# Kernel tuning notes

Hardware: AMD Instinct MI355X
Metric: run time of the kernel (lower is better)

## Reference

```python
import jax, jax.numpy as jnp
import numpy as np

D_MODEL = 1024
NUM_HEADS = 16
HEAD_DIM = D_MODEL // NUM_HEADS
THETA = 10000.0
MAX_SEQ_LEN = 2048
BATCH = 4
SEQ = 2048


def _rope_tables():
    # theta_vec = 1 / theta**(arange(0, d_k, 2)/d_k), pos outer product
    inv_freq = 1.0 / (THETA ** (jnp.arange(0, HEAD_DIM, 2, dtype=jnp.float32) / HEAD_DIM))
    pos = jnp.arange(MAX_SEQ_LEN, dtype=jnp.float32)
    freqs = jnp.outer(pos, inv_freq)  # [max_seq, head_dim//2]
    return jnp.cos(freqs), jnp.sin(freqs)


def apply_rope(x, cos, sin):
    # x: [..., S, d]; cos/sin: [S, d//2]; interleaved pairwise rotation
    x1 = x[..., 0::2]
    x2 = x[..., 1::2]
    o1 = x1 * cos - x2 * sin
    o2 = x2 * cos + x1 * sin
    return jnp.stack([o1, o2], axis=-1).reshape(x.shape)


def setup_inputs() -> dict:
    key = jax.random.key(0)
    kx, kq, kk, kv, ko = jax.random.split(key, 5)
    std = (1.0 / D_MODEL) ** 0.5
    x = jax.random.normal(kx, (BATCH, SEQ, D_MODEL), dtype=jnp.float32)
    w_q = jax.random.normal(kq, (D_MODEL, D_MODEL), dtype=jnp.float32) * std
    w_k = jax.random.normal(kk, (D_MODEL, D_MODEL), dtype=jnp.float32) * std
    w_v = jax.random.normal(kv, (D_MODEL, D_MODEL), dtype=jnp.float32) * std
    w_o = jax.random.normal(ko, (D_MODEL, D_MODEL), dtype=jnp.float32) * std
    cos, sin = _rope_tables()
    return {"x": x, "w_q": w_q, "w_k": w_k, "w_v": w_v, "w_o": w_o,
            "cos": cos, "sin": sin}


def reference(x, w_q, w_k, w_v, w_o, cos, sin):
    b, s, d = x.shape
    h, dk = NUM_HEADS, HEAD_DIM

    def proj(w):
        # einsum '... s d, hd d -> ... s hd' == x @ w.T, then split heads
        y = jnp.einsum('bsd,ed->bse', x, w)
        return y.reshape(b, s, h, dk).transpose(0, 2, 1, 3)  # [b,h,s,dk]

    q = apply_rope(proj(w_q), cos[:s], sin[:s])
    k = apply_rope(proj(w_k), cos[:s], sin[:s])
    v = proj(w_v)

    scores = jnp.einsum('bhnd,bhmd->bhnm', q, k) / (dk ** 0.5)
    causal = jnp.tril(jnp.ones((s, s), dtype=bool))
    scores = jnp.where(causal, scores, -jnp.inf)
    attn = jax.nn.softmax(scores, axis=-1)
    out = jnp.einsum('bhnm,bhmd->bhnd', attn, v)  # [b,h,s,dk]
    out = out.transpose(0, 2, 1, 3).reshape(b, s, d)
    # einsum '... s hd, d hd -> ... s d' == out @ w_o.T
    return jnp.einsum('bse,de->bsd', out, w_o)
```

## Files before the change

kernel.cpp:

```cpp
#include <hip/hip_runtime.h>
#include <hip/hip_bf16.h>


typedef __bf16 bf16;
typedef __bf16 bf16x8 __attribute__((ext_vector_type(8)));
typedef __bf16 bf16x4 __attribute__((ext_vector_type(4)));
typedef float f32x4 __attribute__((ext_vector_type(4)));

#define LOG2E 1.4426950408889634f
#define ATTN_C1 (0.125f * LOG2E)
#define ATTN_C2 (16.0f * LOG2E)

__device__ __forceinline__ void async16(const void* g, void* l) {
  __builtin_amdgcn_global_load_lds(
      (const __attribute__((address_space(1))) void*)g,
      (__attribute__((address_space(3))) void*)l, 16, 0, 0);
}

__global__ void cast_all_kernel(const float* __restrict__ x,
                                const float* __restrict__ wq,
                                const float* __restrict__ wk,
                                const float* __restrict__ wv,
                                const float* __restrict__ wo,
                                bf16* __restrict__ xb, bf16* __restrict__ wb) {
  int i = blockIdx.x * blockDim.x + threadIdx.x;
  const float* src;
  bf16* dst;
  long o;
  if (i < 2097152) {
    src = x; dst = xb; o = i;
  } else {
    long j = i - 2097152;
    int w = (int)(j >> 18);
    o = j & 262143;
    src = (w == 0) ? wq : (w == 1) ? wk : (w == 2) ? wv : wo;
    dst = wb + (long)w * 1048576;
  }
  float4 v = reinterpret_cast<const float4*>(src)[o];
  bf16x4 out;
  out.x = (bf16)v.x; out.y = (bf16)v.y; out.z = (bf16)v.z; out.w = (bf16)v.w;
  *reinterpret_cast<bf16x4*>(dst + o * 4) = out;
}

template <int EPI>
__global__ __launch_bounds__(256) void gemm_bt(const bf16* __restrict__ A,
                                               const bf16* __restrict__ B,
                                               void* __restrict__ C, int M,
                                               int N, int K) {
  __shared__ __align__(16) bf16 As[128 * 32];
  __shared__ __align__(16) bf16 Bs[128 * 32];
  const int tid = threadIdx.x;
  const int wid = tid >> 6, lane = tid & 63;
  const int quad = lane >> 4, l15 = lane & 15;
  const int waveM = wid >> 1, waveN = wid & 1;
  const int bm = blockIdx.y, bn = blockIdx.x;

  f32x4 acc[4][4] = {};

  const bf16* Ag = A + (long)bm * 128 * K;
  const bf16* Bg = B + (long)bn * 128 * K;

  for (int k0 = 0; k0 < K; k0 += 32) {
#pragma unroll
    for (int it = 0; it < 2; ++it) {
      int chunk = it * 256 + tid;
      int r = chunk >> 2;
      int c = ((chunk & 3) ^ (r & 3)) << 3;
      int ldsbase = (it * 256 + wid * 64) * 16;
      async16(Ag + (long)r * K + k0 + c, (char*)As + ldsbase);
      async16(Bg + (long)r * K + k0 + c, (char*)Bs + ldsbase);
    }
    __syncthreads();
    bf16x8 af[4], bfr[4];
#pragma unroll
    for (int t = 0; t < 4; ++t) {
      int rowA = waveM * 64 + t * 16 + l15;
      af[t] = *(const bf16x8*)(As + rowA * 32 + ((quad ^ (rowA & 3)) << 3));
    }
#pragma unroll
    for (int t = 0; t < 4; ++t) {
      int rowB = waveN * 64 + t * 16 + l15;
      bfr[t] = *(const bf16x8*)(Bs + rowB * 32 + ((quad ^ (rowB & 3)) << 3));
    }
#pragma unroll
    for (int mt = 0; mt < 4; ++mt)
#pragma unroll
      for (int nt = 0; nt < 4; ++nt)
        acc[mt][nt] = __builtin_amdgcn_mfma_f32_16x16x32_bf16(
            af[mt], bfr[nt], acc[mt][nt], 0, 0, 0);
    __syncthreads();
  }

#pragma unroll
  for (int mt = 0; mt < 4; ++mt)
#pragma unroll
    for (int nt = 0; nt < 4; ++nt)
#pragma unroll
      for (int r = 0; r < 4; ++r) {
        int row = bm * 128 + waveM * 64 + mt * 16 + quad * 4 + r;
        int col = bn * 128 + waveN * 64 + nt * 16 + l15;
        float v = acc[mt][nt][r];
        if (EPI == 1) {
          long off = (long)(col >> 11) * 2097152 + (long)row * 2048 +
                     (col & 2047);
          ((bf16*)C)[off] = (bf16)v;
        } else {
          ((float*)C)[(long)row * N + col] = v;
        }
      }
}

__global__ __launch_bounds__(256) void gemm_qk(const bf16* __restrict__ A,
                                               const bf16* __restrict__ B,
                                               bf16* __restrict__ QK,
                                               const float* __restrict__ cosT,
                                               const float* __restrict__ sinT,
                                               int K) {
  __shared__ __align__(16) bf16 As[128 * 32];
  __shared__ __align__(16) bf16 Bs[128 * 32];
  const int tid = threadIdx.x;
  const int wid = tid >> 6, lane = tid & 63;
  const int quad = lane >> 4, l15 = lane & 15;
  const int waveM = wid >> 1, waveN = wid & 1;
  const int bm = blockIdx.y, bn = blockIdx.x;

  f32x4 acc[4][4] = {};
  const bf16* Ag = A + (long)bm * 128 * K;
  const bf16* Bg = B + (long)bn * 128 * K;

  for (int k0 = 0; k0 < K; k0 += 32) {
#pragma unroll
    for (int it = 0; it < 2; ++it) {
      int chunk = it * 256 + tid;
      int r = chunk >> 2;
      int c = ((chunk & 3) ^ (r & 3)) << 3;
      int ldsbase = (it * 256 + wid * 64) * 16;
      async16(Ag + (long)r * K + k0 + c, (char*)As + ldsbase);
      async16(Bg + (long)r * K + k0 + c, (char*)Bs + ldsbase);
    }
    __syncthreads();
    bf16x8 af[4], bfr[4];
#pragma unroll
    for (int t = 0; t < 4; ++t) {
      int rowA = waveM * 64 + t * 16 + l15;
      af[t] = *(const bf16x8*)(As + rowA * 32 + ((quad ^ (rowA & 3)) << 3));
    }
#pragma unroll
    for (int t = 0; t < 4; ++t) {
      int rowB = waveN * 64 + t * 16 + l15;
      bfr[t] = *(const bf16x8*)(Bs + rowB * 32 + ((quad ^ (rowB & 3)) << 3));
    }
#pragma unroll
    for (int mt = 0; mt < 4; ++mt)
#pragma unroll
      for (int nt = 0; nt < 4; ++nt)
        acc[mt][nt] = __builtin_amdgcn_mfma_f32_16x16x32_bf16(
            af[mt], bfr[nt], acc[mt][nt], 0, 0, 0);
    __syncthreads();
  }

#pragma unroll
  for (int mt = 0; mt < 4; ++mt)
#pragma unroll
    for (int nt = 0; nt < 4; ++nt)
#pragma unroll
      for (int r = 0; r < 4; ++r) {
        int row = bm * 128 + waveM * 64 + mt * 16 + quad * 4 + r;
        int col = bn * 128 + waveN * 64 + nt * 16 + l15;
        float v = acc[mt][nt][r];
        float pr = __shfl_xor(v, 1);
        int d = col & 63;
        int ti = (row & 2047) * 32 + (d >> 1);
        float c = cosT[ti], sn = sinT[ti];
        float o = (col & 1) ? (v * c + pr * sn) : (v * c - pr * sn);
        long off = (long)(col >> 10) * 8388608 +
                   (long)(((row >> 11) << 4) + ((col >> 6) & 15)) * 131072 +
                   (long)(row & 2047) * 64 + d;
        QK[off] = (bf16)o;
      }
}

__device__ __forceinline__ void attn_step(const bf16* Ks, const bf16* Vs,
                                          bf16* Pw, const bf16x8* qf,
                                          f32x4* accO, float& lsum, int quad,
                                          int l15, int qloc, bool diag) {
  const int sw = l15 & 7;
  f32x4 sacc[4] = {};
#pragma unroll
  for (int mt = 0; mt < 4; ++mt)
#pragma unroll
    for (int kk = 0; kk < 2; ++kk) {
      bf16x8 kf = *(const bf16x8*)(Ks + (mt * 16 + l15) * 64 +
                                   ((((kk << 2) + quad) ^ sw) << 3));
      sacc[mt] =
          __builtin_amdgcn_mfma_f32_16x16x32_bf16(kf, qf[kk], sacc[mt], 0, 0, 0);
    }
  if (diag) {
#pragma unroll
    for (int mt = 0; mt < 4; ++mt)
#pragma unroll
      for (int r = 0; r < 4; ++r)
        if ((mt * 16 + quad * 4 + r) > qloc) sacc[mt][r] = -__builtin_inff();
  }
  bf16x4 pk[4];
#pragma unroll
  for (int mt = 0; mt < 4; ++mt)
#pragma unroll
    for (int r = 0; r < 4; ++r) {
      float p = exp2f(fmaf(sacc[mt][r], ATTN_C1, -ATTN_C2));
      lsum += p;
      pk[mt][r] = (bf16)p;
    }
#pragma unroll
  for (int mt = 0; mt < 4; ++mt)
    *(bf16x4*)(Pw + l15 * 88 + mt * 16 + quad * 4) = pk[mt];
  asm volatile("s_waitcnt lgkmcnt(0)" ::: "memory");
  bf16x8 pfr[2];
#pragma unroll
  for (int kk = 0; kk < 2; ++kk)
    pfr[kk] = *(const bf16x8*)(Pw + l15 * 88 + kk * 32 + quad * 8);
#pragma unroll
  for (int nt = 0; nt < 4; ++nt)
#pragma unroll
    for (int kk = 0; kk < 2; ++kk) {
      bf16x8 vf = *(const bf16x8*)(Vs + (nt * 16 + l15) * 64 +
                                   ((((kk << 2) + quad) ^ sw) << 3));
      accO[nt] =
          __builtin_amdgcn_mfma_f32_16x16x32_bf16(pfr[kk], vf, accO[nt], 0, 0, 0);
    }
}

__global__ __launch_bounds__(256, 4) void attn_kernel(
    const bf16* __restrict__ Q, const bf16* __restrict__ Kg,
    const bf16* __restrict__ VT, bf16* __restrict__ Out) {
  __shared__ __align__(16) bf16 Ks[64 * 64];
  __shared__ __align__(16) bf16 Vs[64 * 64];
  __shared__ __align__(16) bf16 Ps[4][16 * 88];
  const int tid = threadIdx.x, wid = tid >> 6, lane = tid & 63;
  const int quad = lane >> 4, l15 = lane & 15;
  const int p = blockIdx.x, bh = blockIdx.y;
  const int q0t = p, q1t = 31 - p;
  const bf16* Qb = Q + (long)bh * 131072;
  const bf16* Kb = Kg + (long)bh * 131072;
  const bf16* Vb = VT + (long)bh * 131072;
  bf16* Pw = &Ps[wid][0];
  const int qloc = wid * 16 + l15;

  bf16x8 qf0[2], qf1[2];
#pragma unroll
  for (int kk = 0; kk < 2; ++kk) {
    qf0[kk] = *(const bf16x8*)(Qb + (long)(q0t * 64 + qloc) * 64 + kk * 32 +
                               quad * 8);
    qf1[kk] = *(const bf16x8*)(Qb + (long)(q1t * 64 + qloc) * 64 + kk * 32 +
                               quad * 8);
  }
  f32x4 acc0[4] = {}, acc1[4] = {};
  float l0 = 0.f, l1 = 0.f;

  for (int kt = 0; kt <= q1t; ++kt) {
#pragma unroll
    for (int it = 0; it < 2; ++it) {
      int chunk = it * 256 + tid;
      int r = chunk >> 3;
      int c = (((chunk & 7) ^ (r & 7)) << 3);
      int ldsbase = (it * 256 + wid * 64) * 16;
      async16(Kb + (long)(kt * 64 + r) * 64 + c, (char*)Ks + ldsbase);
      async16(Vb + (long)r * 2048 + kt * 64 + c, (char*)Vs + ldsbase);
    }
    __syncthreads();
    attn_step(Ks, Vs, Pw, qf1, acc1, l1, quad, l15, qloc, kt == q1t);
    if (kt <= q0t)
      attn_step(Ks, Vs, Pw, qf0, acc0, l0, quad, l15, qloc, kt == q0t);
    __syncthreads();
  }

  l0 += __shfl_xor(l0, 16); l0 += __shfl_xor(l0, 32);
  l1 += __shfl_xor(l1, 16); l1 += __shfl_xor(l1, 32);
  float rl0 = 1.0f / l0, rl1 = 1.0f / l1;

  const int b = bh >> 4, h = bh & 15;
#pragma unroll
  for (int r = 0; r < 4; ++r) {
    float lr0 = __shfl(rl0, quad * 4 + r);
    float lr1 = __shfl(rl1, quad * 4 + r);
#pragma unroll
    for (int nt = 0; nt < 4; ++nt) {
      int d = h * 64 + nt * 16 + l15;
      int qg0 = q0t * 64 + wid * 16 + quad * 4 + r;
      int qg1 = q1t * 64 + wid * 16 + quad * 4 + r;
      Out[(long)(b * 2048 + qg0) * 1024 + d] = (bf16)(acc0[nt][r] * lr0);
      Out[(long)(b * 2048 + qg1) * 1024 + d] = (bf16)(acc1[nt][r] * lr1);
    }
  }
}

extern "C" void kernel_launch(void* const* d_in, const int* in_sizes, int n_in,
                              void* d_out, int out_size, void* d_ws,
                              size_t ws_size, hipStream_t stream) {
  const float* x = (const float*)d_in[0];
  const float* w_q = (const float*)d_in[1];
  const float* w_k = (const float*)d_in[2];
  const float* w_v = (const float*)d_in[3];
  const float* w_o = (const float*)d_in[4];
  const float* cosT = (const float*)d_in[5];
  const float* sinT = (const float*)d_in[6];

  char* ws = (char*)d_ws;
  bf16* xb = (bf16*)(ws + 0);
  bf16* wqb = (bf16*)(ws + 16777216);
  bf16* wvb = (bf16*)(ws + 20971520);
  bf16* wob = (bf16*)(ws + 23068672);
  bf16* Qb = (bf16*)(ws + 25165824);
  bf16* Kb = (bf16*)(ws + 41943040);
  bf16* VTb = (bf16*)(ws + 58720256);
  bf16* attnb = xb;

  cast_all_kernel<<<12288, 256, 0, stream>>>(x, w_q, w_k, w_v, w_o, xb, wqb);

  gemm_qk<<<dim3(16, 64), 256, 0, stream>>>(xb, wqb, Qb, cosT, sinT, 1024);
  gemm_bt<1><<<dim3(64, 8), 256, 0, stream>>>(wvb, xb, VTb, 1024, 8192, 1024);

  attn_kernel<<<dim3(16, 64), 256, 0, stream>>>(Qb, Kb, VTb, attnb);

  gemm_bt<2><<<dim3(8, 64), 256, 0, stream>>>(attnb, wob, (float*)d_out, 8192,
                                              1024, 1024);
}
```

Baseline: 290.5 us.

## Double-buffer attention K/V tiles, fuse dual Q-tile steps, shrink GEMM tiles

The attention loop now double-buffers the K/V tiles in LDS, issuing the async load for the next tile before computing the current one. This removes one barrier per iteration and overlaps global loads with MFMA work. The two query tiles share each K fragment load, and the P scratch buffer is shrunk to 64 columns with an XOR swizzle instead of padding. The V and output-projection GEMMs move to a templated kernel with smaller 64x128 and 128x64 tiles, which doubles the block count and improves CU fill. The cost is more LDS per attention block, which may reduce occupancy, and more per-block overhead in the GEMMs.

```diff
diff --git a/kernel.cpp b/kernel.cpp
--- a/kernel.cpp
+++ b/kernel.cpp
@@ -16,6 +16,8 @@
       (const __attribute__((address_space(1))) void*)g,
       (__attribute__((address_space(3))) void*)l, 16, 0, 0);
 }
+
+#define MFMA16(a, b, c) __builtin_amdgcn_mfma_f32_16x16x32_bf16(a, b, c, 0, 0, 0)
 
 __global__ void cast_all_kernel(const float* __restrict__ x,
                                 const float* __restrict__ wq,
@@ -42,63 +44,71 @@
   *reinterpret_cast<bf16x4*>(dst + o * 4) = out;
 }
 
-template <int EPI>
-__global__ __launch_bounds__(256) void gemm_bt(const bf16* __restrict__ A,
-                                               const bf16* __restrict__ B,
-                                               void* __restrict__ C, int M,
-                                               int N, int K) {
-  __shared__ __align__(16) bf16 As[128 * 32];
-  __shared__ __align__(16) bf16 Bs[128 * 32];
+template <int EPI, int TM, int TN>
+__global__ __launch_bounds__(256) void gemm_tile(const bf16* __restrict__ A,
+                                                 const bf16* __restrict__ B,
+                                                 void* __restrict__ C, int N,
+                                                 int K) {
+  constexpr int WM = TM / 64;
+  constexpr int WN = 4 / WM;
+  constexpr int CW = TN / WN;
+  constexpr int NT = CW / 16;
+  constexpr int ROUNDS = (TM + TN) / 64;
+  __shared__ __align__(16) bf16 As[TM * 32];
+  __shared__ __align__(16) bf16 Bs[TN * 32];
   const int tid = threadIdx.x;
   const int wid = tid >> 6, lane = tid & 63;
   const int quad = lane >> 4, l15 = lane & 15;
-  const int waveM = wid >> 1, waveN = wid & 1;
+  const int waveM = wid / WN, waveN = wid % WN;
   const int bm = blockIdx.y, bn = blockIdx.x;
 
-  f32x4 acc[4][4] = {};
-
-  const bf16* Ag = A + (long)bm * 128 * K;
-  const bf16* Bg = B + (long)bn * 128 * K;
+  f32x4 acc[4][NT] = {};
+
+  const bf16* Ag = A + (long)bm * TM * K;
+  const bf16* Bg = B + (long)bn * TN * K;
 
   for (int k0 = 0; k0 < K; k0 += 32) {
 #pragma unroll
-    for (int it = 0; it < 2; ++it) {
-      int chunk = it * 256 + tid;
-      int r = chunk >> 2;
-      int c = ((chunk & 3) ^ (r & 3)) << 3;
-      int ldsbase = (it * 256 + wid * 64) * 16;
-      async16(Ag + (long)r * K + k0 + c, (char*)As + ldsbase);
-      async16(Bg + (long)r * K + k0 + c, (char*)Bs + ldsbase);
-    }
-    __syncthreads();
-    bf16x8 af[4], bfr[4];
+    for (int ri = 0; ri < ROUNDS; ++ri) {
+      int c = ri * 256 + tid;
+      int g = ri * 256 + (wid << 6);
+      bool isA = g < TM * 4;
+      int cl = isA ? c : c - TM * 4;
+      int r = cl >> 2;
+      int col = ((cl & 3) ^ (r & 3)) << 3;
+      const bf16* src = (isA ? Ag : Bg) + (long)r * K + k0 + col;
+      char* dst = isA ? ((char*)As + (long)g * 16)
+                      : ((char*)Bs + (long)(g - TM * 4) * 16);
+      async16(src, dst);
+    }
+    __syncthreads();
+    bf16x8 af[4], bfr[NT];
 #pragma unroll
     for (int t = 0; t < 4; ++t) {
       int rowA = waveM * 64 + t * 16 + l15;
       af[t] = *(const bf16x8*)(As + rowA * 32 + ((quad ^ (rowA & 3)) << 3));
     }
 #pragma unroll
-    for (int t = 0; t < 4; ++t) {
-      int rowB = waveN * 64 + t * 16 + l15;
+    for (int t = 0; t < NT; ++t) {
+      int rowB = waveN * CW + t * 16 + l15;
       bfr[t] = *(const bf16x8*)(Bs + rowB * 32 + ((quad ^ (rowB & 3)) << 3));
     }
 #pragma unroll
     for (int mt = 0; mt < 4; ++mt)
 #pragma unroll
-      for (int nt = 0; nt < 4; ++nt)
-        acc[mt][nt] = __builtin_amdgcn_mfma_f32_16x16x32_bf16(
-            af[mt], bfr[nt], acc[mt][nt], 0, 0, 0);
+      for (int nt = 0; nt < NT; ++nt)
+        acc[mt][nt] = MFMA16(af[mt], bfr[nt], acc[mt][nt]);
     __syncthreads();
   }
 
 #pragma unroll
   for (int mt = 0; mt < 4; ++mt)
 #pragma unroll
-    for (int nt = 0; nt < 4; ++nt)
+    for (int nt = 0; nt < NT; ++nt)
 #pragma unroll
       for (int r = 0; r < 4; ++r) {
-        int row = bm * 128 + waveM * 64 + mt * 16 + quad * 4 + r;
-        int col = bn * 128 + waveN * 64 + nt * 16 + l15;
+        int row = bm * TM + waveM * 64 + mt * 16 + quad * 4 + r;
+        int col = bn * TN + waveN * CW + nt * 16 + l15;
         float v = acc[mt][nt][r];
         if (EPI == 1) {
           long off = (long)(col >> 11) * 2097152 + (long)row * 2048 +
@@ -154,8 +164,7 @@
     for (int mt = 0; mt < 4; ++mt)
 #pragma unroll
       for (int nt = 0; nt < 4; ++nt)
-        acc[mt][nt] = __builtin_amdgcn_mfma_f32_16x16x32_bf16(
-            af[mt], bfr[nt], acc[mt][nt], 0, 0, 0);
+        acc[mt][nt] = MFMA16(af[mt], bfr[nt], acc[mt][nt]);
     __syncthreads();
   }
 
@@ -180,62 +189,12 @@
       }
 }
 
-__device__ __forceinline__ void attn_step(const bf16* Ks, const bf16* Vs,
-                                          bf16* Pw, const bf16x8* qf,
-                                          f32x4* accO, float& lsum, int quad,
-                                          int l15, int qloc, bool diag) {
-  const int sw = l15 & 7;
-  f32x4 sacc[4] = {};
-#pragma unroll
-  for (int mt = 0; mt < 4; ++mt)
-#pragma unroll
-    for (int kk = 0; kk < 2; ++kk) {
-      bf16x8 kf = *(const bf16x8*)(Ks + (mt * 16 + l15) * 64 +
-                                   ((((kk << 2) + quad) ^ sw) << 3));
-      sacc[mt] =
-          __builtin_amdgcn_mfma_f32_16x16x32_bf16(kf, qf[kk], sacc[mt], 0, 0, 0);
-    }
-  if (diag) {
-#pragma unroll
-    for (int mt = 0; mt < 4; ++mt)
-#pragma unroll
-      for (int r = 0; r < 4; ++r)
-        if ((mt * 16 + quad * 4 + r) > qloc) sacc[mt][r] = -__builtin_inff();
-  }
-  bf16x4 pk[4];
-#pragma unroll
-  for (int mt = 0; mt < 4; ++mt)
-#pragma unroll
-    for (int r = 0; r < 4; ++r) {
-      float p = exp2f(fmaf(sacc[mt][r], ATTN_C1, -ATTN_C2));
-      lsum += p;
-      pk[mt][r] = (bf16)p;
-    }
-#pragma unroll
-  for (int mt = 0; mt < 4; ++mt)
-    *(bf16x4*)(Pw + l15 * 88 + mt * 16 + quad * 4) = pk[mt];
-  asm volatile("s_waitcnt lgkmcnt(0)" ::: "memory");
-  bf16x8 pfr[2];
-#pragma unroll
-  for (int kk = 0; kk < 2; ++kk)
-    pfr[kk] = *(const bf16x8*)(Pw + l15 * 88 + kk * 32 + quad * 8);
-#pragma unroll
-  for (int nt = 0; nt < 4; ++nt)
-#pragma unroll
-    for (int kk = 0; kk < 2; ++kk) {
-      bf16x8 vf = *(const bf16x8*)(Vs + (nt * 16 + l15) * 64 +
-                                   ((((kk << 2) + quad) ^ sw) << 3));
-      accO[nt] =
-          __builtin_amdgcn_mfma_f32_16x16x32_bf16(pfr[kk], vf, accO[nt], 0, 0, 0);
-    }
-}
-
 __global__ __launch_bounds__(256, 4) void attn_kernel(
     const bf16* __restrict__ Q, const bf16* __restrict__ Kg,
     const bf16* __restrict__ VT, bf16* __restrict__ Out) {
-  __shared__ __align__(16) bf16 Ks[64 * 64];
-  __shared__ __align__(16) bf16 Vs[64 * 64];
-  __shared__ __align__(16) bf16 Ps[4][16 * 88];
+  __shared__ __align__(16) bf16 Ks[2][64 * 64];
+  __shared__ __align__(16) bf16 Vs[2][64 * 64];
+  __shared__ __align__(16) bf16 Ps[4][16 * 64];
   const int tid = threadIdx.x, wid = tid >> 6, lane = tid & 63;
   const int quad = lane >> 4, l15 = lane & 15;
   const int p = blockIdx.x, bh = blockIdx.y;
@@ -245,6 +204,8 @@
   const bf16* Vb = VT + (long)bh * 131072;
   bf16* Pw = &Ps[wid][0];
   const int qloc = wid * 16 + l15;
+  const int sw = l15 & 7;
+  const int psw = (l15 & 7) << 3;
 
   bf16x8 qf0[2], qf1[2];
 #pragma unroll
@@ -257,21 +218,120 @@
   f32x4 acc0[4] = {}, acc1[4] = {};
   float l0 = 0.f, l1 = 0.f;
 
-  for (int kt = 0; kt <= q1t; ++kt) {
+  auto stage = [&](int kt, int b) {
 #pragma unroll
     for (int it = 0; it < 2; ++it) {
       int chunk = it * 256 + tid;
       int r = chunk >> 3;
       int c = (((chunk & 7) ^ (r & 7)) << 3);
       int ldsbase = (it * 256 + wid * 64) * 16;
-      async16(Kb + (long)(kt * 64 + r) * 64 + c, (char*)Ks + ldsbase);
-      async16(Vb + (long)r * 2048 + kt * 64 + c, (char*)Vs + ldsbase);
-    }
-    __syncthreads();
-    attn_step(Ks, Vs, Pw, qf1, acc1, l1, quad, l15, qloc, kt == q1t);
-    if (kt <= q0t)
-      attn_step(Ks, Vs, Pw, qf0, acc0, l0, quad, l15, qloc, kt == q0t);
-    __syncthreads();
+      async16(Kb + (long)(kt * 64 + r) * 64 + c, (char*)Ks[b] + ldsbase);
+      async16(Vb + (long)r * 2048 + kt * 64 + c, (char*)Vs[b] + ldsbase);
+    }
+  };
+
+  stage(0, 0);
+  int cur = 0;
+  for (int kt = 0; kt <= q1t; ++kt, cur ^= 1) {
+    __syncthreads();
+    if (kt < q1t) stage(kt + 1, cur ^ 1);
+    const bf16* Kc = Ks[cur];
+    const bf16* Vc = Vs[cur];
+    const bool dual = (kt <= q0t);
+
+    f32x4 s1[4] = {}, s0[4] = {};
+    if (dual) {
+#pragma unroll
+      for (int mt = 0; mt < 4; ++mt)
+#pragma unroll
+        for (int kk = 0; kk < 2; ++kk) {
+          bf16x8 kf = *(const bf16x8*)(Kc + (mt * 16 + l15) * 64 +
+                                       ((((kk << 2) + quad) ^ sw) << 3));
+          s1[mt] = MFMA16(kf, qf1[kk], s1[mt]);
+          s0[mt] = MFMA16(kf, qf0[kk], s0[mt]);
+        }
+    } else {
+#pragma unroll
+      for (int mt = 0; mt < 4; ++mt)
+#pragma unroll
+        for (int kk = 0; kk < 2; ++kk) {
+          bf16x8 kf = *(const bf16x8*)(Kc + (mt * 16 + l15) * 64 +
+                                       ((((kk << 2) + quad) ^ sw) << 3));
+          s1[mt] = MFMA16(kf, qf1[kk], s1[mt]);
+        }
+    }
+    if (kt == q1t) {
+#pragma unroll
+      for (int mt = 0; mt < 4; ++mt)
+#pragma unroll
+        for (int r = 0; r < 4; ++r)
+          if ((mt * 16 + quad * 4 + r) > qloc) s1[mt][r] = -__builtin_inff();
+    }
+    if (dual && kt == q0t) {
+#pragma unroll
+      for (int mt = 0; mt < 4; ++mt)
+#pragma unroll
+        for (int r = 0; r < 4; ++r)
+          if ((mt * 16 + quad * 4 + r) > qloc) s0[mt][r] = -__builtin_inff();
+    }
+
+    bf16x4 pk1[4], pk0[4];
+#pragma unroll
+    for (int mt = 0; mt < 4; ++mt)
+#pragma unroll
+      for (int r = 0; r < 4; ++r) {
+        float pv = exp2f(fmaf(s1[mt][r], ATTN_C1, -ATTN_C2));
+        l1 += pv;
+        pk1[mt][r] = (bf16)pv;
+      }
+    if (dual) {
+#pragma unroll
+      for (int mt = 0; mt < 4; ++mt)
+#pragma unroll
+        for (int r = 0; r < 4; ++r) {
+          float pv = exp2f(fmaf(s0[mt][r], ATTN_C1, -ATTN_C2));
+          l0 += pv;
+          pk0[mt][r] = (bf16)pv;
+        }
+    }
+
+#pragma unroll
+    for (int mt = 0; mt < 4; ++mt)
+      *(bf16x4*)(Pw + l15 * 64 + ((mt * 16 + quad * 4) ^ psw)) = pk1[mt];
+    asm volatile("s_waitcnt lgkmcnt(0)" ::: "memory");
+    bf16x8 pf1[2];
+#pragma unroll
+    for (int kk = 0; kk < 2; ++kk)
+      pf1[kk] = *(const bf16x8*)(Pw + l15 * 64 + ((kk * 32 + quad * 8) ^ psw));
+    if (dual) {
+#pragma unroll
+      for (int mt = 0; mt < 4; ++mt)
+        *(bf16x4*)(Pw + l15 * 64 + ((mt * 16 + quad * 4) ^ psw)) = pk0[mt];
+    }
+#pragma unroll
+    for (int nt = 0; nt < 4; ++nt)
+#pragma unroll
+      for (int kk = 0; kk < 2; ++kk) {
+        bf16x8 vf = *(const bf16x8*)(Vc + (nt * 16 + l15) * 64 +
+                                     ((((kk << 2) + quad) ^ sw) << 3));
+        acc1[nt] = MFMA16(pf1[kk], vf, acc1[nt]);
+      }
+    if (dual) {
+      asm volatile("s_waitcnt lgkmcnt(0)" ::: "memory");
+      bf16x8 pf0[2];
+#pragma unroll
+      for (int kk = 0; kk < 2; ++kk)
+        pf0[kk] =
+            *(const bf16x8*)(Pw + l15 * 64 + ((kk * 32 + quad * 8) ^ psw));
+#pragma unroll
+      for (int nt = 0; nt < 4; ++nt)
+#pragma unroll
+        for (int kk = 0; kk < 2; ++kk) {
+          bf16x8 vf = *(const bf16x8*)(Vc + (nt * 16 + l15) * 64 +
+                                       ((((kk << 2) + quad) ^ sw) << 3));
+          acc0[nt] = MFMA16(pf0[kk], vf, acc0[nt]);
+        }
+    }
   }
 
   l0 += __shfl_xor(l0, 16); l0 += __shfl_xor(l0, 32);
@@ -318,10 +378,12 @@
   cast_all_kernel<<<12288, 256, 0, stream>>>(x, w_q, w_k, w_v, w_o, xb, wqb);
 
   gemm_qk<<<dim3(16, 64), 256, 0, stream>>>(xb, wqb, Qb, cosT, sinT, 1024);
-  gemm_bt<1><<<dim3(64, 8), 256, 0, stream>>>(wvb, xb, VTb, 1024, 8192, 1024);
+  gemm_tile<1, 64, 128><<<dim3(64, 16), 256, 0, stream>>>(wvb, xb, VTb, 8192,
+                                                          1024);
 
   attn_kernel<<<dim3(16, 64), 256, 0, stream>>>(Qb, Kb, VTb, attnb);
 
-  gemm_bt<2><<<dim3(8, 64), 256, 0, stream>>>(attnb, wob, (float*)d_out, 8192,
-                                              1024, 1024);
-}
+  gemm_tile<2, 128, 64><<<dim3(16, 64), 256, 0, stream>>>(attnb, wob,
+                                                          (float*)d_out, 1024,
+                                                          1024);
+}
```

New measurement: 294.2 us. No clear change (+1.3%).

## Replace softmax exp with bit-trick exponent, MFMA row sums, smaller GEMM tiles

Applied to the files above, without the earlier changes.

Q is pre-scaled by 2^23·log2e/8 in the QK projection epilogue, and the score accumulator is seeded with a bias constant. The float-to-int conversion of each score then directly yields the bit pattern of an approximate exp2, so the exp2f and fmaf calls per score are dropped and the bf16 packing becomes a byte permute. Row sums are now computed by an extra MFMA of P against a ones vector instead of scalar adds and cross-lane shuffles. The V and output projection GEMMs move to 64x128 and 128x64 tiles so they launch twice as many blocks. The Schraudolph-style exponent approximation adds error and relies on scores staying within a bounded range.

```diff
diff --git a/kernel.cpp b/kernel.cpp
--- a/kernel.cpp
+++ b/kernel.cpp
@@ -8,14 +8,16 @@
 typedef float f32x4 __attribute__((ext_vector_type(4)));
 
 #define LOG2E 1.4426950408889634f
-#define ATTN_C1 (0.125f * LOG2E)
-#define ATTN_C2 (16.0f * LOG2E)
+#define QSCALE (0.125f * LOG2E * 8388608.0f)
+#define SEXP_SEED ((126.94269504f - 16.0f * LOG2E) * 8388608.0f)
 
 __device__ __forceinline__ void async16(const void* g, void* l) {
   __builtin_amdgcn_global_load_lds(
       (const __attribute__((address_space(1))) void*)g,
       (__attribute__((address_space(3))) void*)l, 16, 0, 0);
 }
+
+#define MFMA16(a, b, c) __builtin_amdgcn_mfma_f32_16x16x32_bf16(a, b, c, 0, 0, 0)
 
 __global__ void cast_all_kernel(const float* __restrict__ x,
                                 const float* __restrict__ wq,
@@ -42,63 +44,71 @@
   *reinterpret_cast<bf16x4*>(dst + o * 4) = out;
 }
 
-template <int EPI>
-__global__ __launch_bounds__(256) void gemm_bt(const bf16* __restrict__ A,
-                                               const bf16* __restrict__ B,
-                                               void* __restrict__ C, int M,
-                                               int N, int K) {
-  __shared__ __align__(16) bf16 As[128 * 32];
-  __shared__ __align__(16) bf16 Bs[128 * 32];
+template <int EPI, int TM, int TN>
+__global__ __launch_bounds__(256) void gemm_tile(const bf16* __restrict__ A,
+                                                 const bf16* __restrict__ B,
+                                                 void* __restrict__ C, int N,
+                                                 int K) {
+  constexpr int WM = TM / 64;
+  constexpr int WN = 4 / WM;
+  constexpr int CW = TN / WN;
+  constexpr int NT = CW / 16;
+  constexpr int ROUNDS = (TM + TN) / 64;
+  __shared__ __align__(16) bf16 As[TM * 32];
+  __shared__ __align__(16) bf16 Bs[TN * 32];
   const int tid = threadIdx.x;
   const int wid = tid >> 6, lane = tid & 63;
   const int quad = lane >> 4, l15 = lane & 15;
-  const int waveM = wid >> 1, waveN = wid & 1;
+  const int waveM = wid / WN, waveN = wid % WN;
   const int bm = blockIdx.y, bn = blockIdx.x;
 
-  f32x4 acc[4][4] = {};
-
-  const bf16* Ag = A + (long)bm * 128 * K;
-  const bf16* Bg = B + (long)bn * 128 * K;
+  f32x4 acc[4][NT] = {};
+
+  const bf16* Ag = A + (long)bm * TM * K;
+  const bf16* Bg = B + (long)bn * TN * K;
 
   for (int k0 = 0; k0 < K; k0 += 32) {
 #pragma unroll
-    for (int it = 0; it < 2; ++it) {
-      int chunk = it * 256 + tid;
-      int r = chunk >> 2;
-      int c = ((chunk & 3) ^ (r & 3)) << 3;
-      int ldsbase = (it * 256 + wid * 64) * 16;
-      async16(Ag + (long)r * K + k0 + c, (char*)As + ldsbase);
-      async16(Bg + (long)r * K + k0 + c, (char*)Bs + ldsbase);
-    }
-    __syncthreads();
-    bf16x8 af[4], bfr[4];
+    for (int ri = 0; ri < ROUNDS; ++ri) {
+      int c = ri * 256 + tid;
+      int g = ri * 256 + (wid << 6);
+      bool isA = g < TM * 4;
+      int cl = isA ? c : c - TM * 4;
+      int r = cl >> 2;
+      int col = ((cl & 3) ^ (r & 3)) << 3;
+      const bf16* src = (isA ? Ag : Bg) + (long)r * K + k0 + col;
+      char* dst = isA ? ((char*)As + (long)g * 16)
+                      : ((char*)Bs + (long)(g - TM * 4) * 16);
+      async16(src, dst);
+    }
+    __syncthreads();
+    bf16x8 af[4], bfr[NT];
 #pragma unroll
     for (int t = 0; t < 4; ++t) {
       int rowA = waveM * 64 + t * 16 + l15;
       af[t] = *(const bf16x8*)(As + rowA * 32 + ((quad ^ (rowA & 3)) << 3));
     }
 #pragma unroll
-    for (int t = 0; t < 4; ++t) {
-      int rowB = waveN * 64 + t * 16 + l15;
+    for (int t = 0; t < NT; ++t) {
+      int rowB = waveN * CW + t * 16 + l15;
       bfr[t] = *(const bf16x8*)(Bs + rowB * 32 + ((quad ^ (rowB & 3)) << 3));
     }
 #pragma unroll
     for (int mt = 0; mt < 4; ++mt)
 #pragma unroll
-      for (int nt = 0; nt < 4; ++nt)
-        acc[mt][nt] = __builtin_amdgcn_mfma_f32_16x16x32_bf16(
-            af[mt], bfr[nt], acc[mt][nt], 0, 0, 0);
+      for (int nt = 0; nt < NT; ++nt)
+        acc[mt][nt] = MFMA16(af[mt], bfr[nt], acc[mt][nt]);
     __syncthreads();
   }
 
 #pragma unroll
   for (int mt = 0; mt < 4; ++mt)
 #pragma unroll
-    for (int nt = 0; nt < 4; ++nt)
+    for (int nt = 0; nt < NT; ++nt)
 #pragma unroll
       for (int r = 0; r < 4; ++r) {
-        int row = bm * 128 + waveM * 64 + mt * 16 + quad * 4 + r;
-        int col = bn * 128 + waveN * 64 + nt * 16 + l15;
+        int row = bm * TM + waveM * 64 + mt * 16 + quad * 4 + r;
+        int col = bn * TN + waveN * CW + nt * 16 + l15;
         float v = acc[mt][nt][r];
         if (EPI == 1) {
           long off = (long)(col >> 11) * 2097152 + (long)row * 2048 +
@@ -154,11 +164,11 @@
     for (int mt = 0; mt < 4; ++mt)
 #pragma unroll
       for (int nt = 0; nt < 4; ++nt)
-        acc[mt][nt] = __builtin_amdgcn_mfma_f32_16x16x32_bf16(
-            af[mt], bfr[nt], acc[mt][nt], 0, 0, 0);
-    __syncthreads();
-  }
-
+        acc[mt][nt] = MFMA16(af[mt], bfr[nt], acc[mt][nt]);
+    __syncthreads();
+  }
+
+  const float qsc = (bn < 8) ? QSCALE : 1.0f;
 #pragma unroll
   for (int mt = 0; mt < 4; ++mt)
 #pragma unroll
@@ -173,6 +183,7 @@
         int ti = (row & 2047) * 32 + (d >> 1);
         float c = cosT[ti], sn = sinT[ti];
         float o = (col & 1) ? (v * c + pr * sn) : (v * c - pr * sn);
+        o *= qsc;
         long off = (long)(col >> 10) * 8388608 +
                    (long)(((row >> 11) << 4) + ((col >> 6) & 15)) * 131072 +
                    (long)(row & 2047) * 64 + d;
@@ -182,38 +193,36 @@
 
 __device__ __forceinline__ void attn_step(const bf16* Ks, const bf16* Vs,
                                           bf16* Pw, const bf16x8* qf,
-                                          f32x4* accO, float& lsum, int quad,
-                                          int l15, int qloc, bool diag) {
+                                          const bf16x8 ones, f32x4* accO,
+                                          f32x4& accL, int quad, int l15,
+                                          int qloc, bool diag) {
   const int sw = l15 & 7;
-  f32x4 sacc[4] = {};
+  const f32x4 seedv = {SEXP_SEED, SEXP_SEED, SEXP_SEED, SEXP_SEED};
+  f32x4 sacc[4] = {seedv, seedv, seedv, seedv};
 #pragma unroll
   for (int mt = 0; mt < 4; ++mt)
 #pragma unroll
     for (int kk = 0; kk < 2; ++kk) {
       bf16x8 kf = *(const bf16x8*)(Ks + (mt * 16 + l15) * 64 +
                                    ((((kk << 2) + quad) ^ sw) << 3));
-      sacc[mt] =
-          __builtin_amdgcn_mfma_f32_16x16x32_bf16(kf, qf[kk], sacc[mt], 0, 0, 0);
+      sacc[mt] = MFMA16(kf, qf[kk], sacc[mt]);
     }
   if (diag) {
 #pragma unroll
     for (int mt = 0; mt < 4; ++mt)
 #pragma unroll
       for (int r = 0; r < 4; ++r)
-        if ((mt * 16 + quad * 4 + r) > qloc) sacc[mt][r] = -__builtin_inff();
-  }
-  bf16x4 pk[4];
-#pragma unroll
-  for (int mt = 0; mt < 4; ++mt)
-#pragma unroll
-    for (int r = 0; r < 4; ++r) {
-      float p = exp2f(fmaf(sacc[mt][r], ATTN_C1, -ATTN_C2));
-      lsum += p;
-      pk[mt][r] = (bf16)p;
-    }
-#pragma unroll
-  for (int mt = 0; mt < 4; ++mt)
-    *(bf16x4*)(Pw + l15 * 88 + mt * 16 + quad * 4) = pk[mt];
+        if ((mt * 16 + quad * 4 + r) > qloc) sacc[mt][r] = 0.0f;
+  }
+#pragma unroll
+  for (int mt = 0; mt < 4; ++mt) {
+    int i0 = (int)sacc[mt][0], i1 = (int)sacc[mt][1];
+    int i2 = (int)sacc[mt][2], i3 = (int)sacc[mt][3];
+    uint2 pk;
+    pk.x = __builtin_amdgcn_perm((unsigned)i1, (unsigned)i0, 0x07060302u);
+    pk.y = __builtin_amdgcn_perm((unsigned)i3, (unsigned)i2, 0x07060302u);
+    *(uint2*)(Pw + l15 * 88 + mt * 16 + quad * 4) = pk;
+  }
   asm volatile("s_waitcnt lgkmcnt(0)" ::: "memory");
   bf16x8 pfr[2];
 #pragma unroll
@@ -225,9 +234,11 @@
     for (int kk = 0; kk < 2; ++kk) {
       bf16x8 vf = *(const bf16x8*)(Vs + (nt * 16 + l15) * 64 +
                                    ((((kk << 2) + quad) ^ sw) << 3));
-      accO[nt] =
-          __builtin_amdgcn_mfma_f32_16x16x32_bf16(pfr[kk], vf, accO[nt], 0, 0, 0);
-    }
+      accO[nt] = MFMA16(pfr[kk], vf, accO[nt]);
+    }
+#pragma unroll
+  for (int kk = 0; kk < 2; ++kk)
+    accL = MFMA16(pfr[kk], ones, accL);
 }
 
 __global__ __launch_bounds__(256, 4) void attn_kernel(
@@ -246,6 +257,10 @@
   bf16* Pw = &Ps[wid][0];
   const int qloc = wid * 16 + l15;
 
+  bf16x8 ones;
+#pragma unroll
+  for (int j = 0; j < 8; ++j) ones[j] = (bf16)1.0f;
+
   bf16x8 qf0[2], qf1[2];
 #pragma unroll
   for (int kk = 0; kk < 2; ++kk) {
@@ -255,7 +270,7 @@
                                quad * 8);
   }
   f32x4 acc0[4] = {}, acc1[4] = {};
-  float l0 = 0.f, l1 = 0.f;
+  f32x4 accL0 = {}, accL1 = {};
 
   for (int kt = 0; kt <= q1t; ++kt) {
 #pragma unroll
@@ -268,21 +283,18 @@
       async16(Vb + (long)r * 2048 + kt * 64 + c, (char*)Vs + ldsbase);
     }
     __syncthreads();
-    attn_step(Ks, Vs, Pw, qf1, acc1, l1, quad, l15, qloc, kt == q1t);
+    attn_step(Ks, Vs, Pw, qf1, ones, acc1, accL1, quad, l15, qloc, kt == q1t);
     if (kt <= q0t)
-      attn_step(Ks, Vs, Pw, qf0, acc0, l0, quad, l15, qloc, kt == q0t);
-    __syncthreads();
-  }
-
-  l0 += __shfl_xor(l0, 16); l0 += __shfl_xor(l0, 32);
-  l1 += __shfl_xor(l1, 16); l1 += __shfl_xor(l1, 32);
-  float rl0 = 1.0f / l0, rl1 = 1.0f / l1;
+      attn_step(Ks, Vs, Pw, qf0, ones, acc0, accL0, quad, l15, qloc,
+                kt == q0t);
+    __syncthreads();
+  }
 
   const int b = bh >> 4, h = bh & 15;
 #pragma unroll
   for (int r = 0; r < 4; ++r) {
-    float lr0 = __shfl(rl0, quad * 4 + r);
-    float lr1 = __shfl(rl1, quad * 4 + r);
+    float lr0 = 1.0f / accL0[r];
+    float lr1 = 1.0f / accL1[r];
 #pragma unroll
     for (int nt = 0; nt < 4; ++nt) {
       int d = h * 64 + nt * 16 + l15;
@@ -318,10 +330,12 @@
   cast_all_kernel<<<12288, 256, 0, stream>>>(x, w_q, w_k, w_v, w_o, xb, wqb);
 
   gemm_qk<<<dim3(16, 64), 256, 0, stream>>>(xb, wqb, Qb, cosT, sinT, 1024);
-  gemm_bt<1><<<dim3(64, 8), 256, 0, stream>>>(wvb, xb, VTb, 1024, 8192, 1024);
+  gemm_tile<1, 64, 128><<<dim3(64, 16), 256, 0, stream>>>(wvb, xb, VTb, 8192,
+                                                          1024);
 
   attn_kernel<<<dim3(16, 64), 256, 0, stream>>>(Qb, Kb, VTb, attnb);
 
-  gemm_bt<2><<<dim3(8, 64), 256, 0, stream>>>(attnb, wob, (float*)d_out, 8192,
-                                              1024, 1024);
-}
+  gemm_tile<2, 128, 64><<<dim3(16, 64), 256, 0, stream>>>(attnb, wob,
+                                                          (float*)d_out, 1024,
+                                                          1024);
+}
```

Result: no change. 284.9 us (-1.9%).
